# Kernel optimization log

Measured on AMD Instinct MI355X. Metric: run time of the kernel, lower is better.

Reference implementation:

```python
import jax, jax.numpy as jnp
import numpy as np

S, B, E, H, M = 1024, 4, 1024, 16, 128  # seq, batch, embed, heads, model_dims (key width)
V = E // H                              # value_dims = 64
_WSCALE = 1.0 / np.sqrt(E)              # keep softmax logits O(1)


def _cplx(re, im):
    return jax.lax.complex(re, im)


def setup_inputs() -> dict:
    key = jax.random.key(0)
    ks = jax.random.split(key, 10)
    n = lambda k, shp: jax.random.normal(k, shp, dtype=jnp.float32)
    w = lambda k, shp: n(k, shp) * np.float32(_WSCALE / np.sqrt(2.0))
    return {
        "logits_re": n(ks[0], (S, B, E)),
        "logits_im": n(ks[1], (S, B, E)),
        "wq_re": w(ks[2], (H, M, E)), "wq_im": w(ks[3], (H, M, E)),
        "wk_re": w(ks[4], (H, M, E)), "wk_im": w(ks[5], (H, M, E)),
        "wv_re": w(ks[6], (H, V, E)), "wv_im": w(ks[7], (H, V, E)),
        "wo_re": w(ks[8], (E, E)),    "wo_im": w(ks[9], (E, E)),
    }


def reference(logits_re, logits_im, wq_re, wq_im, wk_re, wk_im,
              wv_re, wv_im, wo_re, wo_im):
    x = _cplx(logits_re, logits_im)          # (s, b, e) complex64
    wq = _cplx(wq_re, wq_im)                 # (h, m, e)
    wk = _cplx(wk_re, wk_im)
    wv = _cplx(wv_re, wv_im)                 # (h, v, e)
    wo = _cplx(wo_re, wo_im)                 # (e, e)

    q = jnp.einsum('hme,sbe->bhsm', wq, x)   # (b, h, s, m)
    k = jnp.einsum('hme,sbe->bhsm', wk, x)
    v = jnp.einsum('hve,sbe->bhsv', wv, x)   # (b, h, s, v)

    scores = jnp.einsum('bhsm,bhtm->bhst', q, k)         # complex, no conjugation (matches torch matmul)
    amp = jnp.abs(scores)                                # -> float32
    causal = jnp.triu(jnp.ones((S, S), dtype=bool), 1)   # True above diagonal -> masked
    amp = jnp.where(causal, -jnp.inf, amp) / jnp.sqrt(jnp.float32(M))
    attn = jax.nn.softmax(amp, axis=-1).astype(scores.dtype)  # cast back to complex64

    upd = jnp.einsum('bhst,bhtv->bhsv', attn, v)         # (b, h, s, v)
    upd = upd.transpose(2, 0, 1, 3).reshape(S, B, E)     # 's2 b (h v)'
    out = jnp.einsum('sbe,ef->sbf', upd, wo) + x         # residual
    # complex output returned as stacked (real, imag) float32 for harness compatibility
    return jnp.stack([out.real, out.imag])
```

## Files before the change

kernel.cpp:

```cpp
#include <hip/hip_runtime.h>
#include <math.h>

#define S_DIM 1024
#define B_DIM 4
#define E_DIM 1024
#define H_DIM 16
#define M_DIM 128
#define V_DIM 64

typedef __attribute__((ext_vector_type(8))) short short8;
typedef __attribute__((ext_vector_type(4))) float f32x4;
typedef __attribute__((ext_vector_type(4))) int int4v;

__device__ __forceinline__ unsigned short f2bf(float f) {
    union { float f; unsigned u; } v; v.f = f;
    unsigned r = v.u + 0x7FFFu + ((v.u >> 16) & 1u);
    return (unsigned short)(r >> 16);
}

__device__ __forceinline__ void async16(const unsigned short* g, unsigned short* l) {
    __builtin_amdgcn_global_load_lds(
        (const __attribute__((address_space(1))) void*)g,
        (__attribute__((address_space(3))) void*)l,
        16, 0, 0);
}

__global__ __launch_bounds__(256) void convert_all(
    const float* __restrict__ xre,  const float* __restrict__ xim,
    const float* __restrict__ wqre, const float* __restrict__ wqim,
    const float* __restrict__ wkre, const float* __restrict__ wkim,
    const float* __restrict__ wvre, const float* __restrict__ wvim,
    unsigned short* __restrict__ xbre, unsigned short* __restrict__ xbim,
    unsigned short* __restrict__ wbre, unsigned short* __restrict__ wbim)
{
    const int i = blockIdx.x * 256 + threadIdx.x;
    const float *re, *im;
    unsigned short *dr, *di;
    int j;
    if (i < 1048576)      { re = xre;  im = xim;  dr = xbre;               di = xbim;               j = i; }
    else if (i < 1572864) { re = wqre; im = wqim; dr = wbre;               di = wbim;               j = i - 1048576; }
    else if (i < 2097152) { re = wkre; im = wkim; dr = wbre + 2048 * 1024; di = wbim + 2048 * 1024; j = i - 1572864; }
    else                  { re = wvre; im = wvim; dr = wbre + 4096 * 1024; di = wbim + 4096 * 1024; j = i - 2097152; }
    float4 r = ((const float4*)re)[j];
    float4 m = ((const float4*)im)[j];
    ushort4 ro, mo;
    ro.x = f2bf(r.x); ro.y = f2bf(r.y); ro.z = f2bf(r.z); ro.w = f2bf(r.w);
    mo.x = f2bf(m.x); mo.y = f2bf(m.y); mo.z = f2bf(m.z); mo.w = f2bf(m.w);
    ((ushort4*)dr)[j] = ro;
    ((ushort4*)di)[j] = mo;
}

__global__ __launch_bounds__(256) void transpose_wo(
    const float* __restrict__ wore, const float* __restrict__ woim,
    unsigned short* __restrict__ wtre, unsigned short* __restrict__ wtim)
{
    __shared__ float tr[32][33], ti[32][33];
    const int bx = blockIdx.x * 32;
    const int by = blockIdx.y * 32;
    const int tx = threadIdx.x & 31, ty = threadIdx.x >> 5;
    for (int i = ty; i < 32; i += 8) {
        tr[i][tx] = wore[(bx + i) * E_DIM + by + tx];
        ti[i][tx] = woim[(bx + i) * E_DIM + by + tx];
    }
    __syncthreads();
    for (int i = ty; i < 32; i += 8) {
        wtre[(by + i) * E_DIM + bx + tx] = f2bf(tr[tx][i]);
        wtim[(by + i) * E_DIM + bx + tx] = f2bf(ti[tx][i]);
    }
}

__global__ __launch_bounds__(256) void vtrans(
    const unsigned short* __restrict__ vrp, const unsigned short* __restrict__ vip,
    unsigned short* __restrict__ vrt, unsigned short* __restrict__ vit)
{
    __shared__ unsigned short tl[2][64][66];
    const int tid = threadIdx.x;
    const int t0 = blockIdx.x * 64;
    const int bh = blockIdx.y;
    #pragma unroll
    for (int pl = 0; pl < 2; ++pl) {
        const unsigned short* src = pl ? vip : vrp;
        #pragma unroll
        for (int p = 0; p < 2; ++p) {
            const int row = p * 32 + (tid >> 3);
            const int col = (tid & 7) * 8;
            short8 d = *(const short8*)&src[((size_t)bh * S_DIM + t0 + row) * V_DIM + col];
            #pragma unroll
            for (int j = 0; j < 8; ++j) tl[pl][row][col + j] = (unsigned short)d[j];
        }
    }
    __syncthreads();
    #pragma unroll
    for (int pl = 0; pl < 2; ++pl) {
        unsigned short* dst = pl ? vit : vrt;
        #pragma unroll
        for (int p = 0; p < 2; ++p) {
            const int v = p * 32 + (tid >> 3);
            const int tc = (tid & 7) * 8;
            short8 d;
            #pragma unroll
            for (int j = 0; j < 8; ++j) d[j] = (short)tl[pl][tc + j][v];
            *(short8*)&dst[((size_t)bh * V_DIM + v) * S_DIM + t0 + tc] = d;
        }
    }
}

template<int MODE>
__global__ __launch_bounds__(256, 2) void cgemm(
    const unsigned short* __restrict__ Are, const unsigned short* __restrict__ Aim,
    const unsigned short* __restrict__ Bre, const unsigned short* __restrict__ Bim,
    unsigned short* __restrict__ qrp, unsigned short* __restrict__ qip,
    unsigned short* __restrict__ krp, unsigned short* __restrict__ kip,
    unsigned short* __restrict__ vrp, unsigned short* __restrict__ vip,
    const float* __restrict__ xre, const float* __restrict__ xim,
    float* __restrict__ out)
{
    __shared__ __align__(16) unsigned short lds[32768];
    const int tid  = threadIdx.x;
    const int wave = tid >> 6;
    const int lane = tid & 63;
    const int r0 = blockIdx.x * 128;
    const int j0 = blockIdx.y * 128;
    const int wm = (wave >> 1) * 64;
    const int wn = (wave & 1) * 64;

    f32x4 accre[4][4], accim[4][4];
    #pragma unroll
    for (int i = 0; i < 4; ++i)
        #pragma unroll
        for (int j = 0; j < 4; ++j) {
            accre[i][j] = (f32x4){0.f, 0.f, 0.f, 0.f};
            accim[i][j] = (f32x4){0.f, 0.f, 0.f, 0.f};
        }

    const int sr   = tid >> 2;
    const int sc   = (tid & 3) * 8;
    const int scol = ((tid & 3) ^ ((tid >> 3) & 3)) * 8;

    const int fr = lane & 15;
    const int xc = ((lane >> 4) ^ ((lane >> 1) & 3)) * 8;

    #define STAGE(sl, bb) { \
        const int kg = (sl) * 32; \
        unsigned short* b_ = &lds[(bb) * 16384]; \
        const size_t ga0 = (size_t)(r0 + sr) * E_DIM + kg + scol; \
        const size_t ga1 = (size_t)(r0 + 64 + sr) * E_DIM + kg + scol; \
        const size_t gb0 = (size_t)(j0 + sr) * E_DIM + kg + scol; \
        const size_t gb1 = (size_t)(j0 + 64 + sr) * E_DIM + kg + scol; \
        async16(Are + ga0, b_ + sr * 32 + sc); \
        async16(Are + ga1, b_ + (64 + sr) * 32 + sc); \
        async16(Aim + ga0, b_ + 4096 + sr * 32 + sc); \
        async16(Aim + ga1, b_ + 4096 + (64 + sr) * 32 + sc); \
        async16(Bre + gb0, b_ + 8192 + sr * 32 + sc); \
        async16(Bre + gb1, b_ + 8192 + (64 + sr) * 32 + sc); \
        async16(Bim + gb0, b_ + 12288 + sr * 32 + sc); \
        async16(Bim + gb1, b_ + 12288 + (64 + sr) * 32 + sc); }

    STAGE(0, 0)
    asm volatile("s_waitcnt vmcnt(0)" ::: "memory");
    __builtin_amdgcn_s_barrier();

    #pragma unroll 1
    for (int s = 0; s < 32; ++s) {
        if (s < 31) STAGE(s + 1, (s + 1) & 1)

        const unsigned short* buf = &lds[(s & 1) * 16384];
        short8 ar[4], ai[4];
        #pragma unroll
        for (int im = 0; im < 4; ++im) {
            const int ro = (wm + im * 16 + fr) * 32 + xc;
            ar[im] = *(const short8*)&buf[ro];
            ai[im] = *(const short8*)&buf[4096 + ro];
        }
        #pragma unroll
        for (int jn = 0; jn < 4; ++jn) {
            const int ro = (wn + jn * 16 + fr) * 32 + xc;
            const short8 br = *(const short8*)&buf[8192 + ro];
            const short8 bi = *(const short8*)&buf[12288 + ro];
            int4v t = *(int4v*)&bi;
            t = t ^ (int)0x80008000;
            const short8 bin = *(short8*)&t;
            #pragma unroll
            for (int im = 0; im < 4; ++im) {
                accre[im][jn] = __builtin_amdgcn_mfma_f32_16x16x32_bf16(ar[im], br,  accre[im][jn], 0, 0, 0);
                accre[im][jn] = __builtin_amdgcn_mfma_f32_16x16x32_bf16(ai[im], bin, accre[im][jn], 0, 0, 0);
                accim[im][jn] = __builtin_amdgcn_mfma_f32_16x16x32_bf16(ar[im], bi,  accim[im][jn], 0, 0, 0);
                accim[im][jn] = __builtin_amdgcn_mfma_f32_16x16x32_bf16(ai[im], br,  accim[im][jn], 0, 0, 0);
            }
        }

        if (s < 31) {
            asm volatile("s_waitcnt vmcnt(0)" ::: "memory");
            __builtin_amdgcn_s_barrier();
        }
    }
    #undef STAGE

    #pragma unroll
    for (int im = 0; im < 4; ++im) {
        #pragma unroll
        for (int reg = 0; reg < 4; ++reg) {
            const int r = r0 + wm + im * 16 + (lane >> 4) * 4 + reg;
            #pragma unroll
            for (int jn = 0; jn < 4; ++jn) {
                const int j = j0 + wn + jn * 16 + fr;
                const float vr = accre[im][jn][reg];
                const float vi = accim[im][jn][reg];
                if (MODE == 0) {
                    const int s = r >> 2, b = r & 3;
                    if (j < 2048) {
                        const int h = j >> 7, m = j & 127;
                        const size_t off = ((size_t)(b * H_DIM + h) * S_DIM + s) * M_DIM + m;
                        qrp[off] = f2bf(vr); qip[off] = f2bf(vi);
                    } else if (j < 4096) {
                        const int jl = j - 2048, h = jl >> 7, m = jl & 127;
                        const size_t off = ((size_t)(b * H_DIM + h) * S_DIM + s) * M_DIM + m;
                        krp[off] = f2bf(vr); kip[off] = f2bf(vi);
                    } else {
                        const int jl = j - 4096, h = jl >> 6, vv = jl & 63;
                        const size_t off = ((size_t)(b * H_DIM + h) * S_DIM + s) * V_DIM + vv;
                        vrp[off] = f2bf(vr); vip[off] = f2bf(vi);
                    }
                } else {
                    const int idx = r * E_DIM + j;
                    out[idx] = vr + xre[idx];
                    out[S_DIM * B_DIM * E_DIM + idx] = vi + xim[idx];
                }
            }
        }
    }
}

__global__ __launch_bounds__(256, 2) void attn_mfma(
    const unsigned short* __restrict__ qr, const unsigned short* __restrict__ qi,
    const unsigned short* __restrict__ kr, const unsigned short* __restrict__ ki,
    const unsigned short* __restrict__ vrt, const unsigned short* __restrict__ vit,
    unsigned short* __restrict__ updre, unsigned short* __restrict__ updim)
{
    __shared__ __align__(16) unsigned short Ks[2][64][136];
    __shared__ __align__(16) unsigned short Vs[2][64][72];
    __shared__ __align__(16) unsigned short Ps[4][16][80];

    const int tid  = threadIdx.x;
    const int wave = tid >> 6;
    const int lane = tid & 63;
    const int qt = (int)gridDim.x - 1 - blockIdx.x;
    const int bh = blockIdx.y;
    const int q0 = qt * 64;
    const size_t base_qk = (size_t)bh * S_DIM * M_DIM;
    const size_t base_v  = (size_t)bh * V_DIM * S_DIM;

    const int fr = lane & 15;
    const int fg = lane >> 4;
    const int fk = fg * 8;

    const int krow = tid >> 4, kcol = (tid & 15) * 8;
    const int vrow = tid >> 3, vcol = (tid & 7) * 8;

    #pragma unroll
    for (int pl = 0; pl < 2; ++pl) {
        const unsigned short* src = pl ? qi : qr;
        #pragma unroll
        for (int p = 0; p < 4; ++p)
            *(short8*)&Ks[pl][p * 16 + krow][kcol] =
                *(const short8*)&src[base_qk + (size_t)(q0 + p * 16 + krow) * M_DIM + kcol];
    }
    __syncthreads();
    short8 Bqr[4], Bqi[4];
    {
        const int qrow = wave * 16 + fr;
        #pragma unroll
        for (int ks = 0; ks < 4; ++ks) {
            Bqr[ks] = *(const short8*)&Ks[0][qrow][ks * 32 + fk];
            Bqi[ks] = *(const short8*)&Ks[1][qrow][ks * 32 + fk];
        }
    }

    f32x4 Ore[4], Oim[4];
    #pragma unroll
    for (int vt = 0; vt < 4; ++vt) {
        Ore[vt] = (f32x4){0.f, 0.f, 0.f, 0.f};
        Oim[vt] = (f32x4){0.f, 0.f, 0.f, 0.f};
    }
    float mrun = -INFINITY, lrun = 0.f;

    const float scale = 0.088388347648318447f;
    const int qglob = q0 + wave * 16 + fr;

    short8 pk[2][4], pv[2][2];
    #pragma unroll
    for (int pl = 0; pl < 2; ++pl) {
        const unsigned short* src = pl ? ki : kr;
        #pragma unroll
        for (int p = 0; p < 4; ++p)
            pk[pl][p] = *(const short8*)&src[base_qk + (size_t)(p * 16 + krow) * M_DIM + kcol];
    }
    #pragma unroll
    for (int pl = 0; pl < 2; ++pl) {
        const unsigned short* src = pl ? vit : vrt;
        #pragma unroll
        for (int p = 0; p < 2; ++p)
            pv[pl][p] = *(const short8*)&src[base_v + (size_t)(p * 32 + vrow) * S_DIM + vcol];
    }

    for (int t0 = 0; t0 <= q0; t0 += 64) {
        __syncthreads();
        #pragma unroll
        for (int pl = 0; pl < 2; ++pl) {
            #pragma unroll
            for (int p = 0; p < 4; ++p)
                *(short8*)&Ks[pl][p * 16 + krow][kcol] = pk[pl][p];
            #pragma unroll
            for (int p = 0; p < 2; ++p)
                *(short8*)&Vs[pl][p * 32 + vrow][vcol] = pv[pl][p];
        }
        __syncthreads();

        if (t0 + 64 <= q0) {
            const int tn = t0 + 64;
            #pragma unroll
            for (int pl = 0; pl < 2; ++pl) {
                const unsigned short* src = pl ? ki : kr;
                #pragma unroll
                for (int p = 0; p < 4; ++p)
                    pk[pl][p] = *(const short8*)&src[base_qk + (size_t)(tn + p * 16 + krow) * M_DIM + kcol];
            }
            #pragma unroll
            for (int pl = 0; pl < 2; ++pl) {
                const unsigned short* src = pl ? vit : vrt;
                #pragma unroll
                for (int p = 0; p < 2; ++p)
                    pv[pl][p] = *(const short8*)&src[base_v + (size_t)(p * 32 + vrow) * S_DIM + tn + vcol];
            }
        }

        f32x4 Sre[4], Sim[4];
        __builtin_amdgcn_s_setprio(1);
        #pragma unroll
        for (int tt = 0; tt < 4; ++tt) {
            Sre[tt] = (f32x4){0.f, 0.f, 0.f, 0.f};
            Sim[tt] = (f32x4){0.f, 0.f, 0.f, 0.f};
            const int trow = tt * 16 + fr;
            #pragma unroll
            for (int ks = 0; ks < 4; ++ks) {
                const short8 Akr = *(const short8*)&Ks[0][trow][ks * 32 + fk];
                const short8 Aki = *(const short8*)&Ks[1][trow][ks * 32 + fk];
                int4v t = *(int4v*)&Aki;
                t = t ^ (int)0x80008000;
                const short8 Akin = *(short8*)&t;
                Sre[tt] = __builtin_amdgcn_mfma_f32_16x16x32_bf16(Akr,  Bqr[ks], Sre[tt], 0, 0, 0);
                Sre[tt] = __builtin_amdgcn_mfma_f32_16x16x32_bf16(Akin, Bqi[ks], Sre[tt], 0, 0, 0);
                Sim[tt] = __builtin_amdgcn_mfma_f32_16x16x32_bf16(Akr,  Bqi[ks], Sim[tt], 0, 0, 0);
                Sim[tt] = __builtin_amdgcn_mfma_f32_16x16x32_bf16(Aki,  Bqr[ks], Sim[tt], 0, 0, 0);
            }
        }
        __builtin_amdgcn_s_setprio(0);

        float amp[4][4];
        float rowmax = -INFINITY;
        #pragma unroll
        for (int tt = 0; tt < 4; ++tt) {
            #pragma unroll
            for (int r = 0; r < 4; ++r) {
                const int tg = t0 + tt * 16 + fg * 4 + r;
                const float re = Sre[tt][r], im = Sim[tt][r];
                const float a = sqrtf(re * re + im * im) * scale;
                const float av = (tg > qglob) ? -INFINITY : a;
                amp[tt][r] = av;
                rowmax = fmaxf(rowmax, av);
            }
        }
        rowmax = fmaxf(rowmax, __shfl_xor(rowmax, 16));
        rowmax = fmaxf(rowmax, __shfl_xor(rowmax, 32));
        const float nm = fmaxf(mrun, rowmax);
        const float alpha = __expf(mrun - nm);
        mrun = nm;
        float psum = 0.f;
        #pragma unroll
        for (int tt = 0; tt < 4; ++tt) {
            #pragma unroll
            for (int r = 0; r < 4; ++r) {
                const float p = __expf(amp[tt][r] - nm);
                psum += p;
                Ps[wave][fr][tt * 16 + fg * 4 + r] = f2bf(p);
            }
        }
        psum += __shfl_xor(psum, 16);
        psum += __shfl_xor(psum, 32);
        lrun = lrun * alpha + psum;

        #pragma unroll
        for (int vt = 0; vt < 4; ++vt)
            #pragma unroll
            for (int r = 0; r < 4; ++r) { Ore[vt][r] *= alpha; Oim[vt][r] *= alpha; }

        const short8 Bp0 = *(const short8*)&Ps[wave][fr][fk];
        const short8 Bp1 = *(const short8*)&Ps[wave][fr][32 + fk];
        __builtin_amdgcn_s_setprio(1);
        #pragma unroll
        for (int vt = 0; vt < 4; ++vt) {
            const int vr2 = vt * 16 + fr;
            const short8 Ar0 = *(const short8*)&Vs[0][vr2][fk];
            const short8 Ar1 = *(const short8*)&Vs[0][vr2][32 + fk];
            const short8 Ai0 = *(const short8*)&Vs[1][vr2][fk];
            const short8 Ai1 = *(const short8*)&Vs[1][vr2][32 + fk];
            Ore[vt] = __builtin_amdgcn_mfma_f32_16x16x32_bf16(Ar0, Bp0, Ore[vt], 0, 0, 0);
            Ore[vt] = __builtin_amdgcn_mfma_f32_16x16x32_bf16(Ar1, Bp1, Ore[vt], 0, 0, 0);
            Oim[vt] = __builtin_amdgcn_mfma_f32_16x16x32_bf16(Ai0, Bp0, Oim[vt], 0, 0, 0);
            Oim[vt] = __builtin_amdgcn_mfma_f32_16x16x32_bf16(Ai1, Bp1, Oim[vt], 0, 0, 0);
        }
        __builtin_amdgcn_s_setprio(0);
    }

    const int b = bh >> 4, h = bh & 15;
    const float inv = 1.0f / lrun;
    const size_t base = ((size_t)(qglob * B_DIM + b)) * E_DIM + h * V_DIM;
    #pragma unroll
    for (int vt = 0; vt < 4; ++vt) {
        ushort4 pr, pi;
        pr.x = f2bf(Ore[vt][0] * inv); pr.y = f2bf(Ore[vt][1] * inv);
        pr.z = f2bf(Ore[vt][2] * inv); pr.w = f2bf(Ore[vt][3] * inv);
        pi.x = f2bf(Oim[vt][0] * inv); pi.y = f2bf(Oim[vt][1] * inv);
        pi.z = f2bf(Oim[vt][2] * inv); pi.w = f2bf(Oim[vt][3] * inv);
        *(ushort4*)&updre[base + vt * 16 + fg * 4] = pr;
        *(ushort4*)&updim[base + vt * 16 + fg * 4] = pi;
    }
}

extern "C" void kernel_launch(void* const* d_in, const int* in_sizes, int n_in,
                              void* d_out, int out_size, void* d_ws, size_t ws_size,
                              hipStream_t stream) {
    const float* xre  = (const float*)d_in[0];
    const float* xim  = (const float*)d_in[1];
    const float* wqre = (const float*)d_in[2];
    const float* wqim = (const float*)d_in[3];
    const float* wkre = (const float*)d_in[4];
    const float* wkim = (const float*)d_in[5];
    const float* wvre = (const float*)d_in[6];
    const float* wvim = (const float*)d_in[7];
    const float* wore = (const float*)d_in[8];
    const float* woim = (const float*)d_in[9];
    float* out = (float*)d_out;

    char* p = (char*)d_ws;
    const size_t QK = (size_t)B_DIM * H_DIM * S_DIM * M_DIM;
    const size_t VS = (size_t)B_DIM * H_DIM * S_DIM * V_DIM;
    const size_t SBE = (size_t)S_DIM * B_DIM * E_DIM;
    unsigned short* qrw = (unsigned short*)p;  p += QK * 2;
    unsigned short* qiw = (unsigned short*)p;  p += QK * 2;
    unsigned short* krw = (unsigned short*)p;  p += QK * 2;
    unsigned short* kiw = (unsigned short*)p;  p += QK * 2;
    unsigned short* vrw = (unsigned short*)p;  p += VS * 2;
    unsigned short* viw = (unsigned short*)p;  p += VS * 2;
    unsigned short* vrt = (unsigned short*)p;  p += VS * 2;
    unsigned short* vit = (unsigned short*)p;  p += VS * 2;
    unsigned short* updre = (unsigned short*)p; p += SBE * 2;
    unsigned short* updim = (unsigned short*)p; p += SBE * 2;
    unsigned short* xbre  = (unsigned short*)p; p += SBE * 2;
    unsigned short* xbim  = (unsigned short*)p; p += SBE * 2;
    unsigned short* wbre  = (unsigned short*)p; p += (size_t)5120 * E_DIM * 2;
    unsigned short* wbim  = (unsigned short*)p; p += (size_t)5120 * E_DIM * 2;
    unsigned short* wtre  = (unsigned short*)p; p += (size_t)E_DIM * E_DIM * 2;
    unsigned short* wtim  = (unsigned short*)p; p += (size_t)E_DIM * E_DIM * 2;

    convert_all<<<9216, 256, 0, stream>>>(xre, xim, wqre, wqim, wkre, wkim, wvre, wvim,
                                          xbre, xbim, wbre, wbim);
    transpose_wo<<<dim3(32, 32), 256, 0, stream>>>(wore, woim, wtre, wtim);

    cgemm<0><<<dim3(32, 40), 256, 0, stream>>>(xbre, xbim, wbre, wbim,
                                               qrw, qiw, krw, kiw, vrw, viw,
                                               nullptr, nullptr, nullptr);
    vtrans<<<dim3(16, 64), 256, 0, stream>>>(vrw, viw, vrt, vit);
    attn_mfma<<<dim3(16, 64), 256, 0, stream>>>(qrw, qiw, krw, kiw, vrt, vit, updre, updim);
    cgemm<1><<<dim3(32, 8), 256, 0, stream>>>(updre, updim, wtre, wtim,
                                              nullptr, nullptr, nullptr, nullptr, nullptr, nullptr,
                                              xre, xim, out);
}
```

Baseline: 453.8 us.

## Load K/V straight from global in attention, fold scale into Q, lazy rescale

The attention kernel no longer stages Q, K and V through shared memory with register prefetch and block barriers. Each wave now reads its MFMA operands directly from global memory and relies on the cache to serve the reuse across waves. The softmax scale is folded into Q when the projection kernel writes it, and the running-max rescale is skipped unless some row's max grows by more than 8. This removes the LDS traffic and the two syncs per tile, but loses explicit prefetch and exposes global-load latency in the inner loop.

```diff
diff --git a/kernel.cpp b/kernel.cpp
--- a/kernel.cpp
+++ b/kernel.cpp
@@ -196,6 +196,7 @@
     }
     #undef STAGE
 
+    const float qscale = 0.088388347648318447f;
     #pragma unroll
     for (int im = 0; im < 4; ++im) {
         #pragma unroll
@@ -211,7 +212,7 @@
                     if (j < 2048) {
                         const int h = j >> 7, m = j & 127;
                         const size_t off = ((size_t)(b * H_DIM + h) * S_DIM + s) * M_DIM + m;
-                        qrp[off] = f2bf(vr); qip[off] = f2bf(vi);
+                        qrp[off] = f2bf(vr * qscale); qip[off] = f2bf(vi * qscale);
                     } else if (j < 4096) {
                         const int jl = j - 2048, h = jl >> 7, m = jl & 127;
                         const size_t off = ((size_t)(b * H_DIM + h) * S_DIM + s) * M_DIM + m;
@@ -237,9 +238,7 @@
     const unsigned short* __restrict__ vrt, const unsigned short* __restrict__ vit,
     unsigned short* __restrict__ updre, unsigned short* __restrict__ updim)
 {
-    __shared__ __align__(16) unsigned short Ks[2][64][136];
-    __shared__ __align__(16) unsigned short Vs[2][64][72];
-    __shared__ __align__(16) unsigned short Ps[4][16][80];
+    __shared__ __align__(16) unsigned short Ps[4][16][88];
 
     const int tid  = threadIdx.x;
     const int wave = tid >> 6;
@@ -254,25 +253,13 @@
     const int fg = lane >> 4;
     const int fk = fg * 8;
 
-    const int krow = tid >> 4, kcol = (tid & 15) * 8;
-    const int vrow = tid >> 3, vcol = (tid & 7) * 8;
-
-    #pragma unroll
-    for (int pl = 0; pl < 2; ++pl) {
-        const unsigned short* src = pl ? qi : qr;
-        #pragma unroll
-        for (int p = 0; p < 4; ++p)
-            *(short8*)&Ks[pl][p * 16 + krow][kcol] =
-                *(const short8*)&src[base_qk + (size_t)(q0 + p * 16 + krow) * M_DIM + kcol];
-    }
-    __syncthreads();
     short8 Bqr[4], Bqi[4];
     {
-        const int qrow = wave * 16 + fr;
+        const size_t qo = base_qk + (size_t)(q0 + wave * 16 + fr) * M_DIM + fk;
         #pragma unroll
         for (int ks = 0; ks < 4; ++ks) {
-            Bqr[ks] = *(const short8*)&Ks[0][qrow][ks * 32 + fk];
-            Bqi[ks] = *(const short8*)&Ks[1][qrow][ks * 32 + fk];
+            Bqr[ks] = *(const short8*)&qr[qo + ks * 32];
+            Bqi[ks] = *(const short8*)&qi[qo + ks * 32];
         }
     }
 
@@ -283,80 +270,35 @@
         Oim[vt] = (f32x4){0.f, 0.f, 0.f, 0.f};
     }
     float mrun = -INFINITY, lrun = 0.f;
-
-    const float scale = 0.088388347648318447f;
     const int qglob = q0 + wave * 16 + fr;
 
-    short8 pk[2][4], pv[2][2];
-    #pragma unroll
-    for (int pl = 0; pl < 2; ++pl) {
-        const unsigned short* src = pl ? ki : kr;
-        #pragma unroll
-        for (int p = 0; p < 4; ++p)
-            pk[pl][p] = *(const short8*)&src[base_qk + (size_t)(p * 16 + krow) * M_DIM + kcol];
-    }
-    #pragma unroll
-    for (int pl = 0; pl < 2; ++pl) {
-        const unsigned short* src = pl ? vit : vrt;
-        #pragma unroll
-        for (int p = 0; p < 2; ++p)
-            pv[pl][p] = *(const short8*)&src[base_v + (size_t)(p * 32 + vrow) * S_DIM + vcol];
-    }
-
     for (int t0 = 0; t0 <= q0; t0 += 64) {
-        __syncthreads();
-        #pragma unroll
-        for (int pl = 0; pl < 2; ++pl) {
-            #pragma unroll
-            for (int p = 0; p < 4; ++p)
-                *(short8*)&Ks[pl][p * 16 + krow][kcol] = pk[pl][p];
-            #pragma unroll
-            for (int p = 0; p < 2; ++p)
-                *(short8*)&Vs[pl][p * 32 + vrow][vcol] = pv[pl][p];
-        }
-        __syncthreads();
-
-        if (t0 + 64 <= q0) {
-            const int tn = t0 + 64;
-            #pragma unroll
-            for (int pl = 0; pl < 2; ++pl) {
-                const unsigned short* src = pl ? ki : kr;
-                #pragma unroll
-                for (int p = 0; p < 4; ++p)
-                    pk[pl][p] = *(const short8*)&src[base_qk + (size_t)(tn + p * 16 + krow) * M_DIM + kcol];
+        f32x4 Sre[4], Sim[4];
+        #pragma unroll
+        for (int tt = 0; tt < 4; ++tt) {
+            const size_t ko = base_qk + (size_t)(t0 + tt * 16 + fr) * M_DIM + fk;
+            short8 Akr[4], Aki[4];
+            #pragma unroll
+            for (int ks = 0; ks < 4; ++ks) {
+                Akr[ks] = *(const short8*)&kr[ko + ks * 32];
+                Aki[ks] = *(const short8*)&ki[ko + ks * 32];
             }
-            #pragma unroll
-            for (int pl = 0; pl < 2; ++pl) {
-                const unsigned short* src = pl ? vit : vrt;
-                #pragma unroll
-                for (int p = 0; p < 2; ++p)
-                    pv[pl][p] = *(const short8*)&src[base_v + (size_t)(p * 32 + vrow) * S_DIM + tn + vcol];
-            }
-        }
-
-        f32x4 Sre[4], Sim[4];
-        __builtin_amdgcn_s_setprio(1);
-        #pragma unroll
-        for (int tt = 0; tt < 4; ++tt) {
             Sre[tt] = (f32x4){0.f, 0.f, 0.f, 0.f};
             Sim[tt] = (f32x4){0.f, 0.f, 0.f, 0.f};
-            const int trow = tt * 16 + fr;
+            __builtin_amdgcn_s_setprio(1);
             #pragma unroll
             for (int ks = 0; ks < 4; ++ks) {
-                const short8 Akr = *(const short8*)&Ks[0][trow][ks * 32 + fk];
-                const short8 Aki = *(const short8*)&Ks[1][trow][ks * 32 + fk];
-                int4v t = *(int4v*)&Aki;
+                int4v t = *(int4v*)&Aki[ks];
                 t = t ^ (int)0x80008000;
                 const short8 Akin = *(short8*)&t;
-                Sre[tt] = __builtin_amdgcn_mfma_f32_16x16x32_bf16(Akr,  Bqr[ks], Sre[tt], 0, 0, 0);
-                Sre[tt] = __builtin_amdgcn_mfma_f32_16x16x32_bf16(Akin, Bqi[ks], Sre[tt], 0, 0, 0);
-                Sim[tt] = __builtin_amdgcn_mfma_f32_16x16x32_bf16(Akr,  Bqi[ks], Sim[tt], 0, 0, 0);
-                Sim[tt] = __builtin_amdgcn_mfma_f32_16x16x32_bf16(Aki,  Bqr[ks], Sim[tt], 0, 0, 0);
+                Sre[tt] = __builtin_amdgcn_mfma_f32_16x16x32_bf16(Akr[ks], Bqr[ks], Sre[tt], 0, 0, 0);
+                Sre[tt] = __builtin_amdgcn_mfma_f32_16x16x32_bf16(Akin,    Bqi[ks], Sre[tt], 0, 0, 0);
+                Sim[tt] = __builtin_amdgcn_mfma_f32_16x16x32_bf16(Akr[ks], Bqi[ks], Sim[tt], 0, 0, 0);
+                Sim[tt] = __builtin_amdgcn_mfma_f32_16x16x32_bf16(Aki[ks], Bqr[ks], Sim[tt], 0, 0, 0);
             }
-        }
-        __builtin_amdgcn_s_setprio(0);
-
-        float amp[4][4];
+            __builtin_amdgcn_s_setprio(0);
+        }
+
         float rowmax = -INFINITY;
         #pragma unroll
         for (int tt = 0; tt < 4; ++tt) {
@@ -364,46 +306,52 @@
             for (int r = 0; r < 4; ++r) {
                 const int tg = t0 + tt * 16 + fg * 4 + r;
                 const float re = Sre[tt][r], im = Sim[tt][r];
-                const float a = sqrtf(re * re + im * im) * scale;
+                const float a = sqrtf(re * re + im * im);
                 const float av = (tg > qglob) ? -INFINITY : a;
-                amp[tt][r] = av;
+                Sre[tt][r] = av;
                 rowmax = fmaxf(rowmax, av);
             }
         }
         rowmax = fmaxf(rowmax, __shfl_xor(rowmax, 16));
         rowmax = fmaxf(rowmax, __shfl_xor(rowmax, 32));
-        const float nm = fmaxf(mrun, rowmax);
-        const float alpha = __expf(mrun - nm);
-        mrun = nm;
+
+        if (!__all(rowmax - mrun <= 8.0f)) {
+            const float nm = fmaxf(mrun, rowmax);
+            const float alpha = __expf(mrun - nm);
+            mrun = nm;
+            lrun *= alpha;
+            #pragma unroll
+            for (int vt = 0; vt < 4; ++vt)
+                #pragma unroll
+                for (int r = 0; r < 4; ++r) { Ore[vt][r] *= alpha; Oim[vt][r] *= alpha; }
+        }
+
         float psum = 0.f;
         #pragma unroll
         for (int tt = 0; tt < 4; ++tt) {
-            #pragma unroll
-            for (int r = 0; r < 4; ++r) {
-                const float p = __expf(amp[tt][r] - nm);
-                psum += p;
-                Ps[wave][fr][tt * 16 + fg * 4 + r] = f2bf(p);
-            }
+            const float p0 = __expf(Sre[tt][0] - mrun);
+            const float p1 = __expf(Sre[tt][1] - mrun);
+            const float p2 = __expf(Sre[tt][2] - mrun);
+            const float p3 = __expf(Sre[tt][3] - mrun);
+            psum += p0 + p1 + p2 + p3;
+            ushort4 pw;
+            pw.x = f2bf(p0); pw.y = f2bf(p1); pw.z = f2bf(p2); pw.w = f2bf(p3);
+            *(ushort4*)&Ps[wave][fr][tt * 16 + fg * 4] = pw;
         }
         psum += __shfl_xor(psum, 16);
         psum += __shfl_xor(psum, 32);
-        lrun = lrun * alpha + psum;
-
-        #pragma unroll
-        for (int vt = 0; vt < 4; ++vt)
-            #pragma unroll
-            for (int r = 0; r < 4; ++r) { Ore[vt][r] *= alpha; Oim[vt][r] *= alpha; }
+        lrun += psum;
 
         const short8 Bp0 = *(const short8*)&Ps[wave][fr][fk];
         const short8 Bp1 = *(const short8*)&Ps[wave][fr][32 + fk];
         __builtin_amdgcn_s_setprio(1);
         #pragma unroll
         for (int vt = 0; vt < 4; ++vt) {
-            const int vr2 = vt * 16 + fr;
-            const short8 Ar0 = *(const short8*)&Vs[0][vr2][fk];
-            const short8 Ar1 = *(const short8*)&Vs[0][vr2][32 + fk];
-            const short8 Ai0 = *(const short8*)&Vs[1][vr2][fk];
-            const short8 Ai1 = *(const short8*)&Vs[1][vr2][32 + fk];
+            const size_t vo = base_v + (size_t)(vt * 16 + fr) * S_DIM + t0 + fk;
+            const short8 Ar0 = *(const short8*)&vrt[vo];
+            const short8 Ar1 = *(const short8*)&vrt[vo + 32];
+            const short8 Ai0 = *(const short8*)&vit[vo];
+            const short8 Ai1 = *(const short8*)&vit[vo + 32];
             Ore[vt] = __builtin_amdgcn_mfma_f32_16x16x32_bf16(Ar0, Bp0, Ore[vt], 0, 0, 0);
             Ore[vt] = __builtin_amdgcn_mfma_f32_16x16x32_bf16(Ar1, Bp1, Ore[vt], 0, 0, 0);
             Oim[vt] = __builtin_amdgcn_mfma_f32_16x16x32_bf16(Ai0, Bp0, Oim[vt], 0, 0, 0);
```

Result: slower. 673.9 us (+48.5%).

## Fold softmax scale into Q, lazy rescale, vectorized P stores, remap block order

Applied to the files above, without the earlier changes.

Folds the 1/sqrt(M) scale into the Q projection epilogue so the attention loop skips a multiply per score. The online-softmax rescale of O and l now runs only when some row's max grows by more than a threshold (wave-uniform check), otherwise the stale max is kept. P writes to LDS are packed into 4-element stores, with the Ps row padding changed. Blocks are remapped so consecutive blocks cover different heads at the same causal depth, which balances work and locality. The risk is reduced precision, since Q is rounded after scaling and probabilities may reach up to e^8 in bf16 before normalization.

```diff
diff --git a/kernel.cpp b/kernel.cpp
--- a/kernel.cpp
+++ b/kernel.cpp
@@ -196,6 +196,7 @@
     }
     #undef STAGE
 
+    const float qscale = 0.088388347648318447f;
     #pragma unroll
     for (int im = 0; im < 4; ++im) {
         #pragma unroll
@@ -211,7 +212,7 @@
                     if (j < 2048) {
                         const int h = j >> 7, m = j & 127;
                         const size_t off = ((size_t)(b * H_DIM + h) * S_DIM + s) * M_DIM + m;
-                        qrp[off] = f2bf(vr); qip[off] = f2bf(vi);
+                        qrp[off] = f2bf(vr * qscale); qip[off] = f2bf(vi * qscale);
                     } else if (j < 4096) {
                         const int jl = j - 2048, h = jl >> 7, m = jl & 127;
                         const size_t off = ((size_t)(b * H_DIM + h) * S_DIM + s) * M_DIM + m;
@@ -239,13 +240,17 @@
 {
     __shared__ __align__(16) unsigned short Ks[2][64][136];
     __shared__ __align__(16) unsigned short Vs[2][64][72];
-    __shared__ __align__(16) unsigned short Ps[4][16][80];
+    __shared__ __align__(16) unsigned short Ps[4][16][88];
 
     const int tid  = threadIdx.x;
     const int wave = tid >> 6;
     const int lane = tid & 63;
-    const int qt = (int)gridDim.x - 1 - blockIdx.x;
-    const int bh = blockIdx.y;
+
+    const int n  = blockIdx.x + 16 * blockIdx.y;
+    const int m_ = n >> 3;
+    const int bh = (n & 7) + 8 * (m_ >> 4);
+    const int qt = 15 - (m_ & 15);
+
     const int q0 = qt * 64;
     const size_t base_qk = (size_t)bh * S_DIM * M_DIM;
     const size_t base_v  = (size_t)bh * V_DIM * S_DIM;
@@ -283,8 +288,6 @@
         Oim[vt] = (f32x4){0.f, 0.f, 0.f, 0.f};
     }
     float mrun = -INFINITY, lrun = 0.f;
-
-    const float scale = 0.088388347648318447f;
     const int qglob = q0 + wave * 16 + fr;
 
     short8 pk[2][4], pv[2][2];
@@ -356,7 +359,6 @@
         }
         __builtin_amdgcn_s_setprio(0);
 
-        float amp[4][4];
         float rowmax = -INFINITY;
         #pragma unroll
         for (int tt = 0; tt < 4; ++tt) {
@@ -364,35 +366,41 @@
             for (int r = 0; r < 4; ++r) {
                 const int tg = t0 + tt * 16 + fg * 4 + r;
                 const float re = Sre[tt][r], im = Sim[tt][r];
-                const float a = sqrtf(re * re + im * im) * scale;
+                const float a = sqrtf(re * re + im * im);
                 const float av = (tg > qglob) ? -INFINITY : a;
-                amp[tt][r] = av;
+                Sre[tt][r] = av;
                 rowmax = fmaxf(rowmax, av);
             }
         }
         rowmax = fmaxf(rowmax, __shfl_xor(rowmax, 16));
         rowmax = fmaxf(rowmax, __shfl_xor(rowmax, 32));
-        const float nm = fmaxf(mrun, rowmax);
-        const float alpha = __expf(mrun - nm);
-        mrun = nm;
+
+        if (!__all(rowmax - mrun <= 8.0f)) {
+            const float nm = fmaxf(mrun, rowmax);
+            const float alpha = __expf(mrun - nm);
+            mrun = nm;
+            lrun *= alpha;
+            #pragma unroll
+            for (int vt = 0; vt < 4; ++vt)
+                #pragma unroll
+                for (int r = 0; r < 4; ++r) { Ore[vt][r] *= alpha; Oim[vt][r] *= alpha; }
+        }
+
         float psum = 0.f;
         #pragma unroll
         for (int tt = 0; tt < 4; ++tt) {
-            #pragma unroll
-            for (int r = 0; r < 4; ++r) {
-                const float p = __expf(amp[tt][r] - nm);
-                psum += p;
-                Ps[wave][fr][tt * 16 + fg * 4 + r] = f2bf(p);
-            }
+            const float p0 = __expf(Sre[tt][0] - mrun);
+            const float p1 = __expf(Sre[tt][1] - mrun);
+            const float p2 = __expf(Sre[tt][2] - mrun);
+            const float p3 = __expf(Sre[tt][3] - mrun);
+            psum += p0 + p1 + p2 + p3;
+            ushort4 pw;
+            pw.x = f2bf(p0); pw.y = f2bf(p1); pw.z = f2bf(p2); pw.w = f2bf(p3);
+            *(ushort4*)&Ps[wave][fr][tt * 16 + fg * 4] = pw;
         }
         psum += __shfl_xor(psum, 16);
         psum += __shfl_xor(psum, 32);
-        lrun = lrun * alpha + psum;
-
-        #pragma unroll
-        for (int vt = 0; vt < 4; ++vt)
-            #pragma unroll
-            for (int r = 0; r < 4; ++r) { Ore[vt][r] *= alpha; Oim[vt][r] *= alpha; }
+        lrun += psum;
 
         const short8 Bp0 = *(const short8*)&Ps[wave][fr][fk];
         const short8 Bp1 = *(const short8*)&Ps[wave][fr][32 + fk];
```

Measured after the change: 449.9 us. About the same (-0.9%).
